# Optimization experiments

Measured on AMD Instinct MI355X. Metric: run time of the kernel, lower is better.

## Reference

```python
import jax, jax.numpy as jnp
import numpy as np

KSIZE = 5
# OpenCV: sigma=0 -> sigma = 0.3*((ksize-1)*0.5 - 1) + 0.8
SIGMA = 0.3 * ((KSIZE - 1) * 0.5 - 1.0) + 0.8  # = 1.1 for ksize=5


def _gauss_taps(ksize, sigma):
    r = (ksize - 1) / 2.0
    xs = np.arange(ksize, dtype=np.float64) - r
    w = np.exp(-(xs ** 2) / (2.0 * sigma ** 2))
    w /= w.sum()
    return jnp.asarray(w, dtype=jnp.float32)


def setup_inputs() -> dict:
    key = jax.random.key(0)
    x = jax.random.normal(key, (64, 384, 512, 3), dtype=jnp.float32)
    return {"x": x}


def reference(x):
    # Separable 5x5 Gaussian blur, OpenCV default border BORDER_REFLECT_101
    # (numpy/jnp 'reflect' mode, edge pixel not repeated).
    w = _gauss_taps(KSIZE, SIGMA)  # [5]
    pad = KSIZE // 2
    B, H, W, C = x.shape
    # vertical pass
    xp = jnp.pad(x, ((0, 0), (pad, pad), (0, 0), (0, 0)), mode="reflect")
    y = sum(w[k] * xp[:, k:k + H, :, :] for k in range(KSIZE))
    # horizontal pass
    yp = jnp.pad(y, ((0, 0), (0, 0), (pad, pad), (0, 0)), mode="reflect")
    out = sum(w[k] * yp[:, :, k:k + W, :] for k in range(KSIZE))
    return out
```

## Files before the change

### kernel.cpp

```cpp
#include <hip/hip_runtime.h>


#define BN 64
#define HN 384
#define WN 512
#define CN 3
#define ROWF (WN * CN)
#define ROWQ (ROWF / 4)
#define TH 4
#define NTILES (HN / TH)
#define NTHR 512
#define NBLK (BN * NTILES)

#define CW0 0.07076630f
#define CW1 0.24446040f
#define CW2 0.36954650f

typedef float vfloat4 __attribute__((ext_vector_type(4)));

__global__ __launch_bounds__(NTHR, 6) void gauss_blur_fused(
        const float* __restrict__ x, float* __restrict__ out) {
    __shared__ float v[8 * 4 * 256];

    const int bid  = blockIdx.x;
    const int tile = (bid & 7) * (NBLK >> 3) + (bid >> 3);
    const int b    = tile / NTILES;
    const int h0   = (tile - b * NTILES) * TH;
    const float* __restrict__ xb = x + (size_t)b * HN * ROWF;
    float* __restrict__ ob = out + ((size_t)b * HN + h0) * ROWF;

    const int wid = threadIdx.x >> 6;
    const int l   = threadIdx.x & 63;
    const int q0  = wid * 48;
    int c = q0 - 2 + l;
    c = c < 0 ? 0 : (c > ROWQ - 1 ? ROWQ - 1 : c);

    float4 win[8];
#pragma unroll
    for (int i = 0; i < 8; ++i) {
        int hs = h0 + i - 2;
        hs = hs < 0 ? -hs : hs;
        hs = hs >= HN ? 2 * HN - 2 - hs : hs;
        win[i] = ((const float4*)(xb + (size_t)hs * ROWF))[c];
    }

    float* const vw = v + wid * (TH * 256);

#pragma unroll
    for (int r = 0; r < TH; ++r) {
        float4 a;
        a.x = CW0 * (win[r].x + win[r + 4].x) +
              CW1 * (win[r + 1].x + win[r + 3].x) + CW2 * win[r + 2].x;
        a.y = CW0 * (win[r].y + win[r + 4].y) +
              CW1 * (win[r + 1].y + win[r + 3].y) + CW2 * win[r + 2].y;
        a.z = CW0 * (win[r].z + win[r + 4].z) +
              CW1 * (win[r + 1].z + win[r + 3].z) + CW2 * win[r + 2].z;
        a.w = CW0 * (win[r].w + win[r + 4].w) +
              CW1 * (win[r + 1].w + win[r + 3].w) + CW2 * win[r + 2].w;
        ((float4*)(vw + r * 256))[l] = a;
    }

    if (q0 == 0 && l < TH * 6) {
        int r = l / 6, p = l - 6 * r;
        float* vr = vw + r * 256;
        vr[2 + p] = vr[p < 3 ? 14 + p : 8 + p];
    } else if (q0 == 336 && l < TH * 6) {
        int r = l / 6, p = l - 6 * r;
        float* vr = vw + r * 256;
        vr[200 + p] = vr[p < 3 ? 194 + p : 188 + p];
    }

    if (l < 48) {
#pragma unroll
        for (int r = 0; r < TH; ++r) {
            const float* vr = vw + r * 256;
            float wnd[20];
#pragma unroll
            for (int k = 0; k < 5; ++k) {
                float4 t = ((const float4*)vr)[l + k];
                wnd[4 * k + 0] = t.x;
                wnd[4 * k + 1] = t.y;
                wnd[4 * k + 2] = t.z;
                wnd[4 * k + 3] = t.w;
            }
            vfloat4 res;
#pragma unroll
            for (int j = 0; j < 4; ++j) {
                res[j] =
                    CW0 * (wnd[j + 2] + wnd[j + 14]) +
                    CW1 * (wnd[j + 5] + wnd[j + 11]) +
                    CW2 * wnd[j + 8];
            }
            __builtin_nontemporal_store(res,
                &((vfloat4*)ob)[r * ROWQ + q0 + l]);
        }
    }
}

extern "C" void kernel_launch(void* const* d_in, const int* in_sizes, int n_in,
                              void* d_out, int out_size, void* d_ws, size_t ws_size,
                              hipStream_t stream) {
    const float* x = (const float*)d_in[0];
    float* out = (float*)d_out;
    gauss_blur_fused<<<dim3(NBLK), dim3(NTHR), 0, stream>>>(x, out);
}
```

Baseline: 258.6 us.

## Blur horizontally first from shifted unaligned global loads, dropping the LDS stage

The kernel is restructured so each thread owns one float4 column of the row. It does the horizontal pass first, using five overlapping unaligned vector loads per input row read directly from global memory instead of going through shared memory. The vertical pass then runs over a register ring of 12 horizontally-filtered rows to produce 8 output rows per block, with loads software-pipelined two rows ahead using sched barriers. This removes the LDS round trip, the block's shared memory and the edge-fixup pass, and cuts vertical halo overhead from 8 reads per 4 outputs to 12 per 8. In exchange, global read traffic per row rises fivefold (mostly served by cache), and the border lanes need hand-coded reflect formulas, which is error-prone.

```diff
diff --git a/kernel.cpp b/kernel.cpp
--- a/kernel.cpp
+++ b/kernel.cpp
@@ -7,94 +7,108 @@
 #define CN 3
 #define ROWF (WN * CN)
 #define ROWQ (ROWF / 4)
-#define TH 4
-#define NTILES (HN / TH)
-#define NTHR 512
-#define NBLK (BN * NTILES)
+#define TOUT 8
+#define NROWS (TOUT + 4)
+#define NSTR (HN / TOUT)
+#define NT 384
+#define NBLK (BN * NSTR)
 
 #define CW0 0.07076630f
 #define CW1 0.24446040f
 #define CW2 0.36954650f
 
 typedef float vfloat4 __attribute__((ext_vector_type(4)));
+typedef float f4u __attribute__((ext_vector_type(4), aligned(4)));
 
-__global__ __launch_bounds__(NTHR, 6) void gauss_blur_fused(
+__global__ __launch_bounds__(NT, 3) void gauss_blur_fused(
         const float* __restrict__ x, float* __restrict__ out) {
-    __shared__ float v[8 * 4 * 256];
-
-    const int bid  = blockIdx.x;
-    const int tile = (bid & 7) * (NBLK >> 3) + (bid >> 3);
-    const int b    = tile / NTILES;
-    const int h0   = (tile - b * NTILES) * TH;
+    const int bid = blockIdx.x;
+    const int id  = (bid & 7) * (NBLK >> 3) + (bid >> 3);
+    const int b   = id / NSTR;
+    const int h0  = (id - b * NSTR) * TOUT;
     const float* __restrict__ xb = x + (size_t)b * HN * ROWF;
     float* __restrict__ ob = out + ((size_t)b * HN + h0) * ROWF;
+    const int q = threadIdx.x;
 
-    const int wid = threadIdx.x >> 6;
-    const int l   = threadIdx.x & 63;
-    const int q0  = wid * 48;
-    int c = q0 - 2 + l;
-    c = c < 0 ? 0 : (c > ROWQ - 1 ? ROWQ - 1 : c);
-
-    float4 win[8];
+    int off[5];
 #pragma unroll
-    for (int i = 0; i < 8; ++i) {
-        int hs = h0 + i - 2;
-        hs = hs < 0 ? -hs : hs;
-        hs = hs >= HN ? 2 * HN - 2 - hs : hs;
-        win[i] = ((const float4*)(xb + (size_t)hs * ROWF))[c];
+    for (int k = 0; k < 5; ++k) {
+        int o = 4 * q + 3 * k - 6;
+        off[k] = o < 0 ? 0 : (o > ROWF - 4 ? ROWF - 4 : o);
     }
 
-    float* const vw = v + wid * (TH * 256);
+    const float* rp[NROWS];
+#pragma unroll
+    for (int i = 0; i < NROWS; ++i) {
+        int hr = h0 + i - 2;
+        hr = hr < 0 ? -hr : hr;
+        hr = hr >= HN ? 2 * HN - 2 - hr : hr;
+        rp[i] = xb + (size_t)hr * ROWF;
+    }
+
+    vfloat4 t[3][5];
+    vfloat4 h[NROWS];
+
+#define ISSUE(s, i) do { _Pragma("unroll") \
+    for (int k = 0; k < 5; ++k) \
+        t[s][k] = (vfloat4)(*(const f4u*)(rp[i] + off[k])); } while (0)
+
+    ISSUE(0, 0);
+    ISSUE(1, 1);
+    __builtin_amdgcn_sched_barrier(0);
 
 #pragma unroll
-    for (int r = 0; r < TH; ++r) {
-        float4 a;
-        a.x = CW0 * (win[r].x + win[r + 4].x) +
-              CW1 * (win[r + 1].x + win[r + 3].x) + CW2 * win[r + 2].x;
-        a.y = CW0 * (win[r].y + win[r + 4].y) +
-              CW1 * (win[r + 1].y + win[r + 3].y) + CW2 * win[r + 2].y;
-        a.z = CW0 * (win[r].z + win[r + 4].z) +
-              CW1 * (win[r + 1].z + win[r + 3].z) + CW2 * win[r + 2].z;
-        a.w = CW0 * (win[r].w + win[r + 4].w) +
-              CW1 * (win[r + 1].w + win[r + 3].w) + CW2 * win[r + 2].w;
-        ((float4*)(vw + r * 256))[l] = a;
-    }
+    for (int i = 0; i < NROWS; ++i) {
+        if (i + 2 < NROWS) {
+            ISSUE((i + 2) % 3, i + 2);
+            __builtin_amdgcn_sched_barrier(0);
+        }
+        const int s = i % 3;
+        vfloat4 hb = CW0 * (t[s][0] + t[s][4]) +
+                     CW1 * (t[s][1] + t[s][3]) +
+                     CW2 * t[s][2];
+        if (q == 0) {
+            hb[0] = 2*CW0*t[s][4][0] + 2*CW1*t[s][3][0] + CW2*t[s][2][0];
+            hb[1] = 2*CW0*t[s][4][1] + 2*CW1*t[s][3][1] + CW2*t[s][2][1];
+            hb[2] = 2*CW0*t[s][4][2] + 2*CW1*t[s][3][2] + CW2*t[s][2][2];
+            hb[3] = CW0*(t[s][2][3]+t[s][4][3]) + CW1*(t[s][2][0]+t[s][3][3])
+                  + CW2*t[s][2][3];
+        } else if (q == 1) {
+            hb[0] = CW0*(t[s][2][0]+t[s][4][0]) + CW1*(t[s][1][0]+t[s][3][0])
+                  + CW2*t[s][2][0];
+            hb[1] = CW0*(t[s][2][1]+t[s][4][1]) + CW1*(t[s][1][1]+t[s][3][1])
+                  + CW2*t[s][2][1];
+            hb[2] = CW0*(t[s][0][0]+t[s][4][2]) + CW1*(t[s][1][2]+t[s][3][2])
+                  + CW2*t[s][2][2];
+            hb[3] = CW0*(t[s][1][0]+t[s][4][3]) + CW1*(t[s][2][0]+t[s][4][0])
+                  + CW2*t[s][2][3];
+        } else if (q == 382) {
+            hb[0] = CW0*(t[s][0][0]+t[s][4][2]) + CW1*(t[s][1][0]+t[s][3][0])
+                  + CW2*t[s][2][0];
+            hb[1] = CW0*(t[s][0][1]+t[s][4][3]) + CW1*(t[s][1][1]+t[s][3][1])
+                  + CW2*t[s][2][1];
+            hb[2] = CW0*(t[s][0][2]+t[s][2][2]) + CW1*(t[s][1][2]+t[s][3][2])
+                  + CW2*t[s][2][2];
+            hb[3] = CW0*(t[s][0][3]+t[s][3][0]) + CW1*(t[s][2][0]+t[s][4][2])
+                  + CW2*t[s][3][0];
+        } else if (q == 383) {
+            hb[0] = CW0*(t[s][0][0]+t[s][2][0]) + CW1*(t[s][1][0]+t[s][2][3])
+                  + CW2*t[s][2][0];
+            hb[1] = 2*CW0*t[s][0][1] + 2*CW1*t[s][1][1] + CW2*t[s][2][1];
+            hb[2] = 2*CW0*t[s][0][2] + 2*CW1*t[s][1][2] + CW2*t[s][2][2];
+            hb[3] = 2*CW0*t[s][0][3] + 2*CW1*t[s][1][3] + CW2*t[s][2][3];
+        }
+        h[i] = hb;
 
-    if (q0 == 0 && l < TH * 6) {
-        int r = l / 6, p = l - 6 * r;
-        float* vr = vw + r * 256;
-        vr[2 + p] = vr[p < 3 ? 14 + p : 8 + p];
-    } else if (q0 == 336 && l < TH * 6) {
-        int r = l / 6, p = l - 6 * r;
-        float* vr = vw + r * 256;
-        vr[200 + p] = vr[p < 3 ? 194 + p : 188 + p];
-    }
-
-    if (l < 48) {
-#pragma unroll
-        for (int r = 0; r < TH; ++r) {
-            const float* vr = vw + r * 256;
-            float wnd[20];
-#pragma unroll
-            for (int k = 0; k < 5; ++k) {
-                float4 t = ((const float4*)vr)[l + k];
-                wnd[4 * k + 0] = t.x;
-                wnd[4 * k + 1] = t.y;
-                wnd[4 * k + 2] = t.z;
-                wnd[4 * k + 3] = t.w;
-            }
-            vfloat4 res;
-#pragma unroll
-            for (int j = 0; j < 4; ++j) {
-                res[j] =
-                    CW0 * (wnd[j + 2] + wnd[j + 14]) +
-                    CW1 * (wnd[j + 5] + wnd[j + 11]) +
-                    CW2 * wnd[j + 8];
-            }
+        if (i >= 4) {
+            vfloat4 res = CW0 * (h[i - 4] + h[i]) +
+                          CW1 * (h[i - 3] + h[i - 1]) +
+                          CW2 * h[i - 2];
             __builtin_nontemporal_store(res,
-                &((vfloat4*)ob)[r * ROWQ + q0 + l]);
+                &((vfloat4*)ob)[(i - 4) * ROWQ + q]);
         }
     }
+#undef ISSUE
 }
 
 extern "C" void kernel_launch(void* const* d_in, const int* in_sizes, int n_in,
@@ -102,5 +116,5 @@
                               hipStream_t stream) {
     const float* x = (const float*)d_in[0];
     float* out = (float*)d_out;
-    gauss_blur_fused<<<dim3(NBLK), dim3(NTHR), 0, stream>>>(x, out);
+    gauss_blur_fused<<<dim3(NBLK), dim3(NT), 0, stream>>>(x, out);
 }
```

After: 269.1 us. 1.04x slower.
